# Performance work log

Hardware: AMD Instinct MI355X
Metric: run time of the kernel (lower is better)

Reference implementation:

```python
import jax, jax.numpy as jnp
import numpy as np

OUT = 7                # adaptive pool output size (7,7)
SPATIAL_SCALE = 1.0 / 16.0
NEG = jnp.float32(-3.0e38)  # acts as -inf for masked max


def setup_inputs() -> dict:
    key = jax.random.key(0)
    k1, k2, k3, k4, k5, k6 = jax.random.split(key, 6)
    B, C, H, W = 2, 256, 50, 50
    R = 256
    features = jax.random.normal(k1, (B, C, H, W), dtype=jnp.float32)
    # boxes in image coordinates (image = 800x800, stride 16)
    x1 = jax.random.uniform(k2, (R,), minval=0.0, maxval=500.0)
    y1 = jax.random.uniform(k3, (R,), minval=0.0, maxval=500.0)
    bw = jax.random.uniform(k4, (R,), minval=64.0, maxval=296.0)
    bh = jax.random.uniform(k5, (R,), minval=64.0, maxval=296.0)
    rois = jnp.stack([x1, y1, x1 + bw, y1 + bh], axis=1).astype(jnp.float32)  # [R,4]
    roi_indices = jax.random.randint(k6, (R,), 0, B, dtype=jnp.int64)
    return {"features": features, "rois": rois, "roi_indices": roi_indices}


def _roi_pool(features, rois, roi_indices):
    H, W = features.shape[2], features.shape[3]
    ri = (rois * SPATIAL_SCALE).astype(jnp.int32)           # truncation, as np.astype
    x1, y1, x2, y2 = ri[:, 0], ri[:, 1], ri[:, 2], ri[:, 3]
    # NOTE: original code slices features[idx, :, x1:x2, y1:y2] -> x indexes dim H, y indexes dim W
    Lh = x2 - x1                                            # [R]
    Lw = y2 - y1
    p = jnp.arange(OUT)
    # adaptive max pool bin boundaries (torch semantics): start=floor(i*L/OUT), end=ceil((i+1)*L/OUT)
    hstart = x1[:, None] + (p[None, :] * Lh[:, None]) // OUT                   # [R,OUT]
    hend = x1[:, None] + ((p[None, :] + 1) * Lh[:, None] + OUT - 1) // OUT
    wstart = y1[:, None] + (p[None, :] * Lw[:, None]) // OUT
    wend = y1[:, None] + ((p[None, :] + 1) * Lw[:, None] + OUT - 1) // OUT
    hidx = jnp.arange(H)
    widx = jnp.arange(W)
    row_mask = (hidx[None, None, :] >= hstart[:, :, None]) & (hidx[None, None, :] < hend[:, :, None])  # [R,OUT,H]
    col_mask = (widx[None, None, :] >= wstart[:, :, None]) & (widx[None, None, :] < wend[:, :, None])  # [R,OUT,W]

    feat = features[roi_indices]                            # [R,C,H,W]
    # reduce over W per output column (fixed small loop over OUT bins)
    cols = []
    for pw in range(OUT):
        m = col_mask[:, pw][:, None, None, :]               # [R,1,1,W]
        cols.append(jnp.max(jnp.where(m, feat, NEG), axis=3))  # [R,C,H]
    t = jnp.stack(cols, axis=-1)                            # [R,C,H,OUT]
    # reduce over H per output row
    rows = []
    for ph in range(OUT):
        m = row_mask[:, ph][:, None, :, None]               # [R,1,H,1]
        rows.append(jnp.max(jnp.where(m, t, NEG), axis=2))  # [R,C,OUT]
    return jnp.stack(rows, axis=2)                          # [R,C,OUT,OUT]


def reference(features, rois, roi_indices):
    return _roi_pool(features, rois, roi_indices)
```

## Files before the change

### kernel.cpp

```cpp
#include <hip/hip_runtime.h>
#include <cstddef>
#include <cstdint>


namespace {
constexpr int OUTP = 7;
constexpr int BB = 2;
constexpr int CC = 256;
constexpr int HH = 50;
constexpr int WW = 50;
constexpr int HWSZ = HH * WW;
constexpr int CSPLIT = 2;
constexpr int CPS = CC / CSPLIT;
constexpr float NEGV = -3e38f;
typedef float vf2 __attribute__((ext_vector_type(2)));
}

__global__ __launch_bounds__(256) void transpose_k(const float* __restrict__ in,
                                                   float* __restrict__ out) {
    __shared__ float tile[32][33];
    const int b = blockIdx.z;
    const int hw0 = blockIdx.x * 32;
    const int c0 = blockIdx.y * 32;
    const int tx = threadIdx.x;
#pragma unroll
    for (int i = threadIdx.y; i < 32; i += 8) {
        const int hw = hw0 + tx;
        float v = 0.0f;
        if (hw < HWSZ) v = in[(size_t)(b * CC + c0 + i) * HWSZ + hw];
        tile[i][tx] = v;
    }
    __syncthreads();
    const int ch = c0 + tx;
    const int s = ch >> 7;
    const int cin = ch & (CPS - 1);
#pragma unroll
    for (int i = threadIdx.y; i < 32; i += 8) {
        const int hw = hw0 + i;
        if (hw < HWSZ)
            out[((size_t)((s * BB + b) * HWSZ) + hw) * CPS + cin] = tile[tx][i];
    }
}

__global__ __launch_bounds__(448) void roipool4(const float* __restrict__ feat,
                                                const float* __restrict__ rois,
                                                const int* __restrict__ ridx,
                                                float* __restrict__ out) {
    const int s = blockIdx.x;
    const int r = blockIdx.y;
    const int tid = threadIdx.x;
    const int c2 = tid & 63;
    const int ph = __builtin_amdgcn_readfirstlane(tid >> 6);

    const float4 rv = reinterpret_cast<const float4*>(rois)[r];
    int x1 = (int)(rv.x * 0.0625f);
    int y1 = (int)(rv.y * 0.0625f);
    int x2 = (int)(rv.z * 0.0625f);
    int y2 = (int)(rv.w * 0.0625f);
    int b = ridx[r];
    x1 = __builtin_amdgcn_readfirstlane(x1);
    y1 = __builtin_amdgcn_readfirstlane(y1);
    x2 = __builtin_amdgcn_readfirstlane(x2);
    y2 = __builtin_amdgcn_readfirstlane(y2);
    b = __builtin_amdgcn_readfirstlane(b);

    const int Lh = x2 - x1;
    const int Lw = y2 - y1;

    int hs = x1 + (ph * Lh) / OUTP;
    int he = x1 + ((ph + 1) * Lh + OUTP - 1) / OUTP;
    hs = hs < 0 ? 0 : hs;
    he = he > HH ? HH : he;
    const int nh = he - hs;

    int ws_[OUTP], nw_[OUTP];
    int mx = nh;
#pragma unroll
    for (int p = 0; p < OUTP; ++p) {
        int a = y1 + (p * Lw) / OUTP;
        int e = y1 + ((p + 1) * Lw + OUTP - 1) / OUTP;
        a = a < 0 ? 0 : a;
        e = e > WW ? WW : e;
        ws_[p] = a;
        nw_[p] = e - a;
        mx = mx > (e - a) ? mx : (e - a);
    }

    vf2 acc[OUTP];
#pragma unroll
    for (int p = 0; p < OUTP; ++p) acc[p] = (vf2){NEGV, NEGV};

    const float* base =
        feat + ((size_t)((s * BB + b) * HWSZ) + (size_t)hs * WW) * CPS + 2 * c2;

    if (mx <= 4) {
#pragma unroll
        for (int hh = 0; hh < 4; ++hh) {
            if (hh < nh) {
                const float* rp = base + (size_t)hh * (WW * CPS);
#pragma unroll
                for (int p = 0; p < OUTP; ++p) {
#pragma unroll
                    for (int ww = 0; ww < 4; ++ww) {
                        const int col = ws_[p] + (ww < nw_[p] ? ww : nw_[p] - 1);
                        const vf2 v =
                            *reinterpret_cast<const vf2*>(rp + (size_t)col * CPS);
                        acc[p].x = fmaxf(acc[p].x, v.x);
                        acc[p].y = fmaxf(acc[p].y, v.y);
                    }
                }
            }
        }
    } else {
        for (int hh = 0; hh < nh; ++hh) {
            const float* rp = base + (size_t)hh * (WW * CPS);
#pragma unroll
            for (int p = 0; p < OUTP; ++p) {
                for (int ww = 0; ww < nw_[p]; ++ww) {
                    const vf2 v = *reinterpret_cast<const vf2*>(
                        rp + (size_t)(ws_[p] + ww) * CPS);
                    acc[p].x = fmaxf(acc[p].x, v.x);
                    acc[p].y = fmaxf(acc[p].y, v.y);
                }
            }
        }
    }

    __shared__ float st[CPS * OUTP * OUTP];
#pragma unroll
    for (int p = 0; p < OUTP; ++p) {
        st[(2 * c2) * 49 + ph * OUTP + p] = acc[p].x;
        st[(2 * c2 + 1) * 49 + ph * OUTP + p] = acc[p].y;
    }
    __syncthreads();

    float* ob = out + (size_t)(r * CC + s * CPS) * (OUTP * OUTP);
    const vf2* st2 = reinterpret_cast<const vf2*>(st);
    vf2* ob2 = reinterpret_cast<vf2*>(ob);
#pragma unroll
    for (int k = 0; k < OUTP; ++k) {
        __builtin_nontemporal_store(st2[tid + k * 448], ob2 + tid + k * 448);
    }
}

__global__ __launch_bounds__(256) void roipool_generic(const float* __restrict__ feat,
                                                       const float* __restrict__ rois,
                                                       const int* __restrict__ ridx,
                                                       float* __restrict__ out) {
    const int r = blockIdx.x;
    const int ph = blockIdx.y;
    const int c = threadIdx.x;

    const float4 rv = reinterpret_cast<const float4*>(rois)[r];
    const int x1 = (int)(rv.x * 0.0625f);
    const int y1 = (int)(rv.y * 0.0625f);
    const int x2 = (int)(rv.z * 0.0625f);
    const int y2 = (int)(rv.w * 0.0625f);
    const int b = ridx[r];
    const int Lh = x2 - x1;
    const int Lw = y2 - y1;

    int hs = x1 + (ph * Lh) / OUTP;
    int he = x1 + ((ph + 1) * Lh + OUTP - 1) / OUTP;
    hs = hs < 0 ? 0 : hs;
    he = he > HH ? HH : he;

    float acc[OUTP];
#pragma unroll
    for (int p = 0; p < OUTP; ++p) acc[p] = NEGV;

    for (int h = hs; h < he; ++h) {
#pragma unroll
        for (int p = 0; p < OUTP; ++p) {
            int w0 = y1 + (p * Lw) / OUTP;
            int w1 = y1 + ((p + 1) * Lw + OUTP - 1) / OUTP;
            w0 = w0 < 0 ? 0 : w0;
            w1 = w1 > WW ? WW : w1;
            float m = acc[p];
            for (int w = w0; w < w1; ++w) {
                m = fmaxf(m, feat[((size_t)(b * CC + c) * HH + h) * WW + w]);
            }
            acc[p] = m;
        }
    }

    float* op = out + ((size_t)r * CC + c) * (OUTP * OUTP) + (size_t)ph * OUTP;
#pragma unroll
    for (int p = 0; p < OUTP; ++p) op[p] = acc[p];
}

extern "C" void kernel_launch(void* const* d_in, const int* in_sizes, int n_in,
                              void* d_out, int out_size, void* d_ws, size_t ws_size,
                              hipStream_t stream) {
    const float* features = (const float*)d_in[0];
    const float* rois = (const float*)d_in[1];
    const int* ridx = (const int*)d_in[2];
    float* out = (float*)d_out;
    const int R = in_sizes[1] / 4;

    const size_t tbytes = (size_t)BB * HWSZ * CC * sizeof(float);
    if (ws_size >= tbytes) {
        float* featT = (float*)d_ws;
        dim3 tg((HWSZ + 31) / 32, CC / 32, BB);
        transpose_k<<<tg, dim3(32, 8), 0, stream>>>(features, featT);
        roipool4<<<dim3(CSPLIT, R), 448, 0, stream>>>(featT, rois, ridx, out);
    } else {
        roipool_generic<<<dim3(R, OUTP), 256, 0, stream>>>(features, rois, ridx, out);
    }
}
```

Baseline: 23.15 us.

## Split output columns across two wave sets and specialize bin-size paths

The pooling kernel doubles its block to 896 threads, so 14 waves each handle one output row and a subset of output columns (4 or 3) instead of all 7. Each bin is reduced separately with specialized unrolled paths for widths up to 2 and up to 4, using vector max, and results are written straight to shared memory. The aim is more parallel waves per ROI and less per-thread serial work and register pressure. The cost is duplicated ROI setup per wave, a larger block that may limit occupancy, and an output store done by only half the threads.

```diff
diff --git a/kernel.cpp b/kernel.cpp
--- a/kernel.cpp
+++ b/kernel.cpp
@@ -42,7 +42,7 @@
     }
 }
 
-__global__ __launch_bounds__(448) void roipool4(const float* __restrict__ feat,
+__global__ __launch_bounds__(896) void roipool6(const float* __restrict__ feat,
                                                 const float* __restrict__ rois,
                                                 const int* __restrict__ ridx,
                                                 float* __restrict__ out) {
@@ -50,7 +50,11 @@
     const int r = blockIdx.y;
     const int tid = threadIdx.x;
     const int c2 = tid & 63;
-    const int ph = __builtin_amdgcn_readfirstlane(tid >> 6);
+    const int wv = __builtin_amdgcn_readfirstlane(tid >> 6);
+    const int ph = wv % OUTP;
+    const int bset = wv / OUTP;
+    const int p0 = bset ? 4 : 0;
+    const int np = bset ? 3 : 4;
 
     const float4 rv = reinterpret_cast<const float4*>(rois)[r];
     int x1 = (int)(rv.x * 0.0625f);
@@ -73,73 +77,78 @@
     he = he > HH ? HH : he;
     const int nh = he - hs;
 
-    int ws_[OUTP], nw_[OUTP];
-    int mx = nh;
-#pragma unroll
-    for (int p = 0; p < OUTP; ++p) {
-        int a = y1 + (p * Lw) / OUTP;
-        int e = y1 + ((p + 1) * Lw + OUTP - 1) / OUTP;
-        a = a < 0 ? 0 : a;
-        e = e > WW ? WW : e;
-        ws_[p] = a;
-        nw_[p] = e - a;
-        mx = mx > (e - a) ? mx : (e - a);
-    }
-
-    vf2 acc[OUTP];
-#pragma unroll
-    for (int p = 0; p < OUTP; ++p) acc[p] = (vf2){NEGV, NEGV};
+    __shared__ float st[CPS * OUTP * OUTP];
 
     const float* base =
         feat + ((size_t)((s * BB + b) * HWSZ) + (size_t)hs * WW) * CPS + 2 * c2;
-
-    if (mx <= 4) {
-#pragma unroll
-        for (int hh = 0; hh < 4; ++hh) {
-            if (hh < nh) {
-                const float* rp = base + (size_t)hh * (WW * CPS);
-#pragma unroll
-                for (int p = 0; p < OUTP; ++p) {
-#pragma unroll
-                    for (int ww = 0; ww < 4; ++ww) {
-                        const int col = ws_[p] + (ww < nw_[p] ? ww : nw_[p] - 1);
+    const int rowstride = WW * CPS;
+
+#pragma unroll
+    for (int pi = 0; pi < 4; ++pi) {
+        if (pi < np) {
+            const int p = p0 + pi;
+            int a = y1 + (p * Lw) / OUTP;
+            int e = y1 + ((p + 1) * Lw + OUTP - 1) / OUTP;
+            a = a < 0 ? 0 : a;
+            e = e > WW ? WW : e;
+            const int nw = e - a;
+
+            vf2 m = (vf2){NEGV, NEGV};
+            const float* bp = base + (size_t)a * CPS;
+
+            if (nw <= 2 && nh <= 4) {
+                const int c1 = (nw > 1 ? 1 : 0) * CPS;
+#pragma unroll
+                for (int hh = 0; hh < 4; ++hh) {
+                    if (hh < nh) {
+                        const float* rp = bp + hh * rowstride;
+                        const vf2 v0 = *reinterpret_cast<const vf2*>(rp);
+                        const vf2 v1 = *reinterpret_cast<const vf2*>(rp + c1);
+                        m = __builtin_elementwise_max(m, v0);
+                        m = __builtin_elementwise_max(m, v1);
+                    }
+                }
+            } else if (nw <= 4 && nh <= 4) {
+                const int c3 = (nw - 1) * CPS;
+#pragma unroll
+                for (int hh = 0; hh < 4; ++hh) {
+                    if (hh < nh) {
+                        const float* rp = bp + hh * rowstride;
+                        const vf2 v0 = *reinterpret_cast<const vf2*>(rp);
+                        const vf2 v1 = *reinterpret_cast<const vf2*>(rp + CPS);
+                        const vf2 v2 = *reinterpret_cast<const vf2*>(rp + 2 * CPS);
+                        const vf2 v3 = *reinterpret_cast<const vf2*>(rp + c3);
+                        m = __builtin_elementwise_max(m, v0);
+                        m = __builtin_elementwise_max(m, v1);
+                        m = __builtin_elementwise_max(m, v2);
+                        m = __builtin_elementwise_max(m, v3);
+                    }
+                }
+            } else {
+                for (int hh = 0; hh < nh; ++hh) {
+                    const float* rp = bp + hh * rowstride;
+                    for (int ww = 0; ww < nw; ++ww) {
                         const vf2 v =
-                            *reinterpret_cast<const vf2*>(rp + (size_t)col * CPS);
-                        acc[p].x = fmaxf(acc[p].x, v.x);
-                        acc[p].y = fmaxf(acc[p].y, v.y);
+                            *reinterpret_cast<const vf2*>(rp + (size_t)ww * CPS);
+                        m = __builtin_elementwise_max(m, v);
                     }
                 }
             }
+
+            st[(2 * c2) * 49 + ph * OUTP + p] = m.x;
+            st[(2 * c2 + 1) * 49 + ph * OUTP + p] = m.y;
         }
-    } else {
-        for (int hh = 0; hh < nh; ++hh) {
-            const float* rp = base + (size_t)hh * (WW * CPS);
-#pragma unroll
-            for (int p = 0; p < OUTP; ++p) {
-                for (int ww = 0; ww < nw_[p]; ++ww) {
-                    const vf2 v = *reinterpret_cast<const vf2*>(
-                        rp + (size_t)(ws_[p] + ww) * CPS);
-                    acc[p].x = fmaxf(acc[p].x, v.x);
-                    acc[p].y = fmaxf(acc[p].y, v.y);
-                }
-            }
+    }
+    __syncthreads();
+
+    if (tid < 448) {
+        float* ob = out + (size_t)(r * CC + s * CPS) * (OUTP * OUTP);
+        const vf2* st2 = reinterpret_cast<const vf2*>(st);
+        vf2* ob2 = reinterpret_cast<vf2*>(ob);
+#pragma unroll
+        for (int k = 0; k < OUTP; ++k) {
+            __builtin_nontemporal_store(st2[tid + k * 448], ob2 + tid + k * 448);
         }
-    }
-
-    __shared__ float st[CPS * OUTP * OUTP];
-#pragma unroll
-    for (int p = 0; p < OUTP; ++p) {
-        st[(2 * c2) * 49 + ph * OUTP + p] = acc[p].x;
-        st[(2 * c2 + 1) * 49 + ph * OUTP + p] = acc[p].y;
-    }
-    __syncthreads();
-
-    float* ob = out + (size_t)(r * CC + s * CPS) * (OUTP * OUTP);
-    const vf2* st2 = reinterpret_cast<const vf2*>(st);
-    vf2* ob2 = reinterpret_cast<vf2*>(ob);
-#pragma unroll
-    for (int k = 0; k < OUTP; ++k) {
-        __builtin_nontemporal_store(st2[tid + k * 448], ob2 + tid + k * 448);
     }
 }
 
@@ -203,7 +212,7 @@
         float* featT = (float*)d_ws;
         dim3 tg((HWSZ + 31) / 32, CC / 32, BB);
         transpose_k<<<tg, dim3(32, 8), 0, stream>>>(features, featT);
-        roipool4<<<dim3(CSPLIT, R), 448, 0, stream>>>(featT, rois, ridx, out);
+        roipool6<<<dim3(CSPLIT, R), 896, 0, stream>>>(featT, rois, ridx, out);
     } else {
         roipool_generic<<<dim3(R, OUTP), 256, 0, stream>>>(features, rois, ridx, out);
     }
```

Result: no change. 22.94 us (-0.9%).
